# Optimization experiments

Hardware: AMD Instinct MI355X
Metric: run time of the kernel (lower is better)

## Reference

```python
import jax, jax.numpy as jnp
import numpy as np

B, C, H, W = 8, 256, 48, 48
CR = C // 8  # query/key channel dim of the 1x1 conv projections


def setup_inputs() -> dict:
    key = jax.random.key(0)
    ks = jax.random.split(key, 8)
    s = 0.05  # weight scale
    return {
        "feat_map": jax.random.normal(ks[0], (B, C, H, W), dtype=jnp.float32),
        "w1": jax.random.normal(ks[1], (CR, C), dtype=jnp.float32) * s,
        "b1": jax.random.normal(ks[2], (CR,), dtype=jnp.float32) * s,
        "w2": jax.random.normal(ks[3], (CR, C), dtype=jnp.float32) * s,
        "b2": jax.random.normal(ks[4], (CR,), dtype=jnp.float32) * s,
        "w3": jax.random.normal(ks[5], (C, C), dtype=jnp.float32) * s,
        "b3": jax.random.normal(ks[6], (C,), dtype=jnp.float32) * s,
        "gamma": jnp.asarray(0.1, dtype=jnp.float32),  # torch inits to 0; nonzero for a meaningful baseline
    }


def reference(feat_map, w1, b1, w2, b2, w3, b3, gamma):
    b, c, h, w = feat_map.shape
    n = h * w
    x = feat_map.reshape(b, c, n)                     # [B,C,N]
    # 1x1 convs == per-pixel channel matmuls
    q = jnp.einsum('dc,bcn->bnd', w1, x) + b1         # [B,N,C/8]
    k = jnp.einsum('dc,bcn->bdn', w2, x) + b2[None, :, None]  # [B,C/8,N]
    attn = jax.nn.softmax(jnp.einsum('bnd,bdm->bnm', q, k), axis=-1)  # [B,N,N]
    v = jnp.einsum('dc,bcn->bdn', w3, x) + b3[None, :, None]  # [B,C,N]
    # out[b,c,i] = sum_j v[b,c,j] * attn[b,i,j]  (matches bmm(v, attn^T))
    refine = jnp.einsum('bcj,bij->bci', v, attn).reshape(b, c, h, w)
    return gamma * refine + feat_map
```

## Files before the change

### kernel.cpp

```cpp
#include <hip/hip_runtime.h>
#include <stdint.h>

#define NB  8
#define NC  256
#define NCR 32
#define NSP 2304

typedef __attribute__((ext_vector_type(8))) short short8;
typedef __attribute__((ext_vector_type(4))) float f32x4;
typedef __attribute__((ext_vector_type(4))) unsigned short us4;

__device__ __forceinline__ unsigned short f2bf(float f) {
  union { float f; unsigned u; } a; a.f = f;
  unsigned r = (a.u + 0x7FFFu + ((a.u >> 16) & 1u)) >> 16;
  return (unsigned short)r;
}

typedef __attribute__((address_space(1))) const void* gvoidp;
typedef __attribute__((address_space(3))) void* lvoidp;
#define GLOADLDS16(g, l) __builtin_amdgcn_global_load_lds((gvoidp)(g), (lvoidp)(l), 16, 0, 0)

__global__ __launch_bounds__(256) void k_proj(const float* __restrict__ x,
    const float* __restrict__ w1, const float* __restrict__ b1,
    const float* __restrict__ w2, const float* __restrict__ b2,
    const float* __restrict__ w3, const float* __restrict__ b3,
    unsigned short* __restrict__ Q, unsigned short* __restrict__ K,
    unsigned short* __restrict__ V) {
  __shared__ unsigned short xs[32][264];
  const int n0 = blockIdx.x * 32, b = blockIdx.y;
  const int t = threadIdx.x, lane = t & 63, wave = t >> 6;
  const int col = lane & 15, quad = lane >> 4;
  const float* xb = x + (size_t)b * NC * NSP;
#pragma unroll
  for (int p = 0; p < 8; ++p) {
    const int crow = (t >> 3) + p * 32;
    const int n4 = (t & 7) * 4;
    float4 v = *(const float4*)(xb + (size_t)crow * NSP + n0 + n4);
    xs[n4 + 0][crow] = f2bf(v.x);
    xs[n4 + 1][crow] = f2bf(v.y);
    xs[n4 + 2][crow] = f2bf(v.z);
    xs[n4 + 3][crow] = f2bf(v.w);
  }
  __syncthreads();
  const f32x4 zero4 = {0.f, 0.f, 0.f, 0.f};
  f32x4 acc[5][2];
#pragma unroll
  for (int i = 0; i < 5; ++i)
#pragma unroll
    for (int j = 0; j < 2; ++j) acc[i][j] = zero4;

  for (int kc = 0; kc < 8; ++kc) {
    short8 bf[2];
#pragma unroll
    for (int nt = 0; nt < 2; ++nt)
      bf[nt] = *(const short8*)&xs[nt * 16 + col][kc * 32 + quad * 8];
#pragma unroll
    for (int ml = 0; ml < 5; ++ml) {
      const int m0 = (wave * 5 + ml) * 16;
      const float* wbase; int roff;
      if (m0 < 32)      { wbase = w1; roff = m0; }
      else if (m0 < 64) { wbase = w2; roff = m0 - 32; }
      else              { wbase = w3; roff = m0 - 64; }
      const float* wp = wbase + (size_t)(roff + col) * NC + kc * 32 + quad * 8;
      float4 f0 = *(const float4*)wp;
      float4 f1 = *(const float4*)(wp + 4);
      short8 af;
      af[0] = f2bf(f0.x); af[1] = f2bf(f0.y); af[2] = f2bf(f0.z); af[3] = f2bf(f0.w);
      af[4] = f2bf(f1.x); af[5] = f2bf(f1.y); af[6] = f2bf(f1.z); af[7] = f2bf(f1.w);
#pragma unroll
      for (int nt = 0; nt < 2; ++nt)
        acc[ml][nt] = __builtin_amdgcn_mfma_f32_16x16x32_bf16(af, bf[nt], acc[ml][nt], 0, 0, 0);
    }
  }
#pragma unroll
  for (int ml = 0; ml < 5; ++ml) {
    const int m0 = (wave * 5 + ml) * 16;
    const float* bias;
    if (m0 < 32)      bias = b1 + m0;
    else if (m0 < 64) bias = b2 + (m0 - 32);
    else              bias = b3 + (m0 - 64);
    float bv[4];
#pragma unroll
    for (int r = 0; r < 4; ++r) bv[r] = bias[quad * 4 + r];
    if (m0 < 64) {
      unsigned short* dst = (m0 < 32) ? Q : K;
      const int d0 = (m0 & 31) + quad * 4;
#pragma unroll
      for (int nt = 0; nt < 2; ++nt) {
        const int n = n0 + nt * 16 + col;
        us4 pk;
#pragma unroll
        for (int r = 0; r < 4; ++r) pk[r] = f2bf(acc[ml][nt][r] + bv[r]);
        *(us4*)(dst + ((size_t)b * NSP + n) * NCR + d0) = pk;
      }
    } else {
      const int cbase = m0 - 64 + quad * 4;
#pragma unroll
      for (int nt = 0; nt < 2; ++nt) {
        const int n = n0 + nt * 16 + col;
#pragma unroll
        for (int r = 0; r < 4; ++r)
          V[((size_t)b * NC + cbase + r) * NSP + n] = f2bf(acc[ml][nt][r] + bv[r]);
      }
    }
  }
}

__global__ __launch_bounds__(192) void k_attn(const unsigned short* __restrict__ Q,
    const unsigned short* __restrict__ K, const unsigned short* __restrict__ V,
    const float* __restrict__ feat, const float* __restrict__ gamma,
    float* __restrict__ out) {
  __shared__ __align__(16) char smem[46592];
  unsigned short* Vs = (unsigned short*)smem;
  unsigned short* Ps = (unsigned short*)(smem + 32768);
  const int i0 = blockIdx.x * 48, ch = blockIdx.y * 128, b = blockIdx.z;
  const int t = threadIdx.x, lane = t & 63, wave = t >> 6;
  const int col = lane & 15, quad = lane >> 4;
  const int iw = i0 + wave * 16;
  const unsigned short* Qb = Q + (size_t)b * NSP * NCR;
  const unsigned short* Kb = K + (size_t)b * NSP * NCR;
  const unsigned short* Vb = V + (size_t)b * NC * NSP;
  unsigned short* PsW = Ps + wave * 2304;

  const short8 qa = *(const short8*)(Qb + (size_t)(iw + col) * NCR + quad * 8);
  const f32x4 zero4 = {0.f, 0.f, 0.f, 0.f};
  f32x4 acc[8];
#pragma unroll
  for (int ct = 0; ct < 8; ++ct) acc[ct] = zero4;
  float rs[4] = {0.f, 0.f, 0.f, 0.f};
  const int srow = lane >> 2, sj = (lane & 3) * 8;

  short8 kb[4];
#pragma unroll
  for (int mt = 0; mt < 4; ++mt)
    kb[mt] = *(const short8*)(Kb + (size_t)(mt * 16 + col) * NCR + quad * 8);
#pragma unroll
  for (int cix = 0; cix < 6; ++cix) {
    const int q = wave * 6 + cix;
    if (q < 16) {
      const int kk = q >> 3, cb = (q & 7) * 16;
      const unsigned short* g = Vb + (size_t)(ch + cb + srow) * NSP + kk * 32 + sj;
      GLOADLDS16(g, Vs + kk * 4096 + cb * 32);
    }
  }
#pragma unroll
  for (int mt = 0; mt < 4; ++mt) {
    f32x4 s = __builtin_amdgcn_mfma_f32_16x16x32_bf16(qa, kb[mt], zero4, 0, 0, 0);
#pragma unroll
    for (int r = 0; r < 4; ++r) {
      const float e = __expf(s[r]);
      rs[r] += e;
      PsW[(quad * 4 + r) * 72 + mt * 16 + col] = f2bf(e);
    }
  }

  for (int kc = 0; kc < 36; ++kc) {
    __syncthreads();
    const int bufc = kc & 1, bufn = bufc ^ 1;
    const int j1 = (kc + 1) * 64;
    const bool more = (kc + 1 < 36);
    if (more) {
#pragma unroll
      for (int mt = 0; mt < 4; ++mt)
        kb[mt] = *(const short8*)(Kb + (size_t)(j1 + mt * 16 + col) * NCR + quad * 8);
#pragma unroll
      for (int cix = 0; cix < 6; ++cix) {
        const int q = wave * 6 + cix;
        if (q < 16) {
          const int kk = q >> 3, cb = (q & 7) * 16;
          const unsigned short* g = Vb + (size_t)(ch + cb + srow) * NSP + j1 + kk * 32 + sj;
          GLOADLDS16(g, Vs + bufn * 8192 + kk * 4096 + cb * 32);
        }
      }
    }
    const unsigned short* pwc = PsW + bufc * 1152;
    const unsigned short* vsc = Vs + bufc * 8192;
#pragma unroll
    for (int kk = 0; kk < 2; ++kk) {
      const short8 pa = *(const short8*)(pwc + col * 72 + kk * 32 + quad * 8);
#pragma unroll
      for (int ct = 0; ct < 8; ++ct) {
        const short8 vbf = *(const short8*)(vsc + kk * 4096 + (ct * 16 + col) * 32 + quad * 8);
        acc[ct] = __builtin_amdgcn_mfma_f32_16x16x32_bf16(pa, vbf, acc[ct], 0, 0, 0);
      }
    }
    if (more) {
      unsigned short* pwn = PsW + bufn * 1152;
#pragma unroll
      for (int mt = 0; mt < 4; ++mt) {
        f32x4 s = __builtin_amdgcn_mfma_f32_16x16x32_bf16(qa, kb[mt], zero4, 0, 0, 0);
#pragma unroll
        for (int r = 0; r < 4; ++r) {
          const float e = __expf(s[r]);
          rs[r] += e;
          pwn[(quad * 4 + r) * 72 + mt * 16 + col] = f2bf(e);
        }
      }
    }
  }

#pragma unroll
  for (int off = 1; off < 16; off <<= 1)
#pragma unroll
    for (int r = 0; r < 4; ++r) rs[r] += __shfl_xor(rs[r], off, 64);
  const float g = gamma[0];
  float rinv[4];
#pragma unroll
  for (int r = 0; r < 4; ++r) rinv[r] = g / rs[r];

  const float* fb = feat + (size_t)b * NC * NSP;
  float* ob = out + (size_t)b * NC * NSP;
#pragma unroll
  for (int ct = 0; ct < 8; ++ct) {
    const size_t a0 = (size_t)(ch + ct * 16 + col) * NSP + iw + quad * 4;
    float4 f = *(const float4*)(fb + a0);
    float4 o;
    o.x = acc[ct][0] * rinv[0] + f.x;
    o.y = acc[ct][1] * rinv[1] + f.y;
    o.z = acc[ct][2] * rinv[2] + f.z;
    o.w = acc[ct][3] * rinv[3] + f.w;
    *(float4*)(ob + a0) = o;
  }
}

#define OFF_Q  0UL
#define OFF_K  1179648UL
#define OFF_V  2359296UL

extern "C" void kernel_launch(void* const* d_in, const int* in_sizes, int n_in,
                              void* d_out, int out_size, void* d_ws, size_t ws_size,
                              hipStream_t stream) {
  const float* feat  = (const float*)d_in[0];
  const float* w1    = (const float*)d_in[1];
  const float* b1    = (const float*)d_in[2];
  const float* w2    = (const float*)d_in[3];
  const float* b2    = (const float*)d_in[4];
  const float* w3    = (const float*)d_in[5];
  const float* b3    = (const float*)d_in[6];
  const float* gamma = (const float*)d_in[7];
  float* out = (float*)d_out;
  char* ws = (char*)d_ws;
  unsigned short* Q = (unsigned short*)(ws + OFF_Q);
  unsigned short* K = (unsigned short*)(ws + OFF_K);
  unsigned short* V = (unsigned short*)(ws + OFF_V);

  hipLaunchKernelGGL(k_proj, dim3(72, NB), dim3(256), 0, stream,
                     feat, w1, b1, w2, b2, w3, b3, Q, K, V);
  hipLaunchKernelGGL(k_attn, dim3(48, 2, NB), dim3(192), 0, stream,
                     Q, K, V, feat, gamma, out);
}
```

Measured before the change: 171.0 us.

## Retile attention kernel to 96 queries x 64 channels with XOR-swizzled V tiles

Each wave now handles two 16-row query tiles against 64 channels instead of one tile against 128 channels. Each V fragment read from LDS therefore feeds two MFMAs, halving V LDS traffic per MFMA. The V tile is stored in a new 64-wide row layout with XOR swizzling to avoid LDS bank conflicts. The trade-off is that each block recomputes QK^T and exp for twice as many queries, across four channel blocks instead of two. That doubles the redundant softmax work, in exchange for less LDS use and better V reuse.

```diff
diff --git a/kernel.cpp b/kernel.cpp
--- a/kernel.cpp
+++ b/kernel.cpp
@@ -110,49 +110,55 @@
     const unsigned short* __restrict__ K, const unsigned short* __restrict__ V,
     const float* __restrict__ feat, const float* __restrict__ gamma,
     float* __restrict__ out) {
-  __shared__ __align__(16) char smem[46592];
-  unsigned short* Vs = (unsigned short*)smem;
-  unsigned short* Ps = (unsigned short*)(smem + 32768);
-  const int i0 = blockIdx.x * 48, ch = blockIdx.y * 128, b = blockIdx.z;
+  __shared__ __align__(16) unsigned short smem[22016];
+  unsigned short* Vs = smem;
+  unsigned short* Ps = smem + 8192;
+  const int i0 = blockIdx.x * 96, ch = blockIdx.y * 64, b = blockIdx.z;
   const int t = threadIdx.x, lane = t & 63, wave = t >> 6;
   const int col = lane & 15, quad = lane >> 4;
-  const int iw = i0 + wave * 16;
+  const int iw = i0 + wave * 32;
   const unsigned short* Qb = Q + (size_t)b * NSP * NCR;
   const unsigned short* Kb = K + (size_t)b * NSP * NCR;
   const unsigned short* Vb = V + (size_t)b * NC * NSP;
-  unsigned short* PsW = Ps + wave * 2304;
-
-  const short8 qa = *(const short8*)(Qb + (size_t)(iw + col) * NCR + quad * 8);
+  unsigned short* PsW = Ps + wave * 4608;
+
+  short8 qa[2];
+#pragma unroll
+  for (int it = 0; it < 2; ++it)
+    qa[it] = *(const short8*)(Qb + (size_t)(iw + it * 16 + col) * NCR + quad * 8);
   const f32x4 zero4 = {0.f, 0.f, 0.f, 0.f};
-  f32x4 acc[8];
-#pragma unroll
-  for (int ct = 0; ct < 8; ++ct) acc[ct] = zero4;
-  float rs[4] = {0.f, 0.f, 0.f, 0.f};
-  const int srow = lane >> 2, sj = (lane & 3) * 8;
+  f32x4 acc[2][4];
+#pragma unroll
+  for (int it = 0; it < 2; ++it)
+#pragma unroll
+    for (int ct = 0; ct < 4; ++ct) acc[it][ct] = zero4;
+  float rs[2][4] = {{0.f,0.f,0.f,0.f},{0.f,0.f,0.f,0.f}};
+  const int r8 = lane >> 3, pc = lane & 7, jcs = pc ^ r8;
 
   short8 kb[4];
 #pragma unroll
   for (int mt = 0; mt < 4; ++mt)
     kb[mt] = *(const short8*)(Kb + (size_t)(mt * 16 + col) * NCR + quad * 8);
 #pragma unroll
-  for (int cix = 0; cix < 6; ++cix) {
-    const int q = wave * 6 + cix;
-    if (q < 16) {
-      const int kk = q >> 3, cb = (q & 7) * 16;
-      const unsigned short* g = Vb + (size_t)(ch + cb + srow) * NSP + kk * 32 + sj;
-      GLOADLDS16(g, Vs + kk * 4096 + cb * 32);
-    }
-  }
-#pragma unroll
-  for (int mt = 0; mt < 4; ++mt) {
-    f32x4 s = __builtin_amdgcn_mfma_f32_16x16x32_bf16(qa, kb[mt], zero4, 0, 0, 0);
-#pragma unroll
-    for (int r = 0; r < 4; ++r) {
-      const float e = __expf(s[r]);
-      rs[r] += e;
-      PsW[(quad * 4 + r) * 72 + mt * 16 + col] = f2bf(e);
-    }
-  }
+  for (int cix = 0; cix < 3; ++cix) {
+    const int q = wave * 3 + cix;
+    if (q < 8) {
+      const unsigned short* g = Vb + (size_t)(ch + q * 8 + r8) * NSP + jcs * 8;
+      GLOADLDS16(g, Vs + q * 512);
+    }
+  }
+#pragma unroll
+  for (int it = 0; it < 2; ++it)
+#pragma unroll
+    for (int mt = 0; mt < 4; ++mt) {
+      f32x4 s = __builtin_amdgcn_mfma_f32_16x16x32_bf16(qa[it], kb[mt], zero4, 0, 0, 0);
+#pragma unroll
+      for (int r = 0; r < 4; ++r) {
+        const float e = __expf(s[r]);
+        rs[it][r] += e;
+        PsW[(it * 16 + quad * 4 + r) * 72 + mt * 16 + col] = f2bf(e);
+      }
+    }
 
   for (int kc = 0; kc < 36; ++kc) {
     __syncthreads();
@@ -164,63 +170,75 @@
       for (int mt = 0; mt < 4; ++mt)
         kb[mt] = *(const short8*)(Kb + (size_t)(j1 + mt * 16 + col) * NCR + quad * 8);
 #pragma unroll
-      for (int cix = 0; cix < 6; ++cix) {
-        const int q = wave * 6 + cix;
-        if (q < 16) {
-          const int kk = q >> 3, cb = (q & 7) * 16;
-          const unsigned short* g = Vb + (size_t)(ch + cb + srow) * NSP + j1 + kk * 32 + sj;
-          GLOADLDS16(g, Vs + bufn * 8192 + kk * 4096 + cb * 32);
+      for (int cix = 0; cix < 3; ++cix) {
+        const int q = wave * 3 + cix;
+        if (q < 8) {
+          const unsigned short* g = Vb + (size_t)(ch + q * 8 + r8) * NSP + j1 + jcs * 8;
+          GLOADLDS16(g, Vs + bufn * 4096 + q * 512);
         }
       }
     }
-    const unsigned short* pwc = PsW + bufc * 1152;
-    const unsigned short* vsc = Vs + bufc * 8192;
+    const unsigned short* pwc = PsW + bufc * 2304;
+    const unsigned short* vsc = Vs + bufc * 4096;
 #pragma unroll
     for (int kk = 0; kk < 2; ++kk) {
-      const short8 pa = *(const short8*)(pwc + col * 72 + kk * 32 + quad * 8);
-#pragma unroll
-      for (int ct = 0; ct < 8; ++ct) {
-        const short8 vbf = *(const short8*)(vsc + kk * 4096 + (ct * 16 + col) * 32 + quad * 8);
-        acc[ct] = __builtin_amdgcn_mfma_f32_16x16x32_bf16(pa, vbf, acc[ct], 0, 0, 0);
+      short8 pa[2];
+#pragma unroll
+      for (int it = 0; it < 2; ++it)
+        pa[it] = *(const short8*)(pwc + (it * 16 + col) * 72 + kk * 32 + quad * 8);
+#pragma unroll
+      for (int ct = 0; ct < 4; ++ct) {
+        const short8 vbf = *(const short8*)(vsc + (ct * 16 + col) * 64 +
+                                            (((kk * 4 + quad) ^ (col & 7)) * 8));
+        acc[0][ct] = __builtin_amdgcn_mfma_f32_16x16x32_bf16(pa[0], vbf, acc[0][ct], 0, 0, 0);
+        acc[1][ct] = __builtin_amdgcn_mfma_f32_16x16x32_bf16(pa[1], vbf, acc[1][ct], 0, 0, 0);
       }
     }
     if (more) {
-      unsigned short* pwn = PsW + bufn * 1152;
-#pragma unroll
-      for (int mt = 0; mt < 4; ++mt) {
-        f32x4 s = __builtin_amdgcn_mfma_f32_16x16x32_bf16(qa, kb[mt], zero4, 0, 0, 0);
-#pragma unroll
-        for (int r = 0; r < 4; ++r) {
-          const float e = __expf(s[r]);
-          rs[r] += e;
-          pwn[(quad * 4 + r) * 72 + mt * 16 + col] = f2bf(e);
+      unsigned short* pwn = PsW + bufn * 2304;
+#pragma unroll
+      for (int it = 0; it < 2; ++it)
+#pragma unroll
+        for (int mt = 0; mt < 4; ++mt) {
+          f32x4 s = __builtin_amdgcn_mfma_f32_16x16x32_bf16(qa[it], kb[mt], zero4, 0, 0, 0);
+#pragma unroll
+          for (int r = 0; r < 4; ++r) {
+            const float e = __expf(s[r]);
+            rs[it][r] += e;
+            pwn[(it * 16 + quad * 4 + r) * 72 + mt * 16 + col] = f2bf(e);
+          }
         }
-      }
     }
   }
 
 #pragma unroll
   for (int off = 1; off < 16; off <<= 1)
 #pragma unroll
-    for (int r = 0; r < 4; ++r) rs[r] += __shfl_xor(rs[r], off, 64);
+    for (int it = 0; it < 2; ++it)
+#pragma unroll
+      for (int r = 0; r < 4; ++r) rs[it][r] += __shfl_xor(rs[it][r], off, 64);
   const float g = gamma[0];
-  float rinv[4];
-#pragma unroll
-  for (int r = 0; r < 4; ++r) rinv[r] = g / rs[r];
+  float rinv[2][4];
+#pragma unroll
+  for (int it = 0; it < 2; ++it)
+#pragma unroll
+    for (int r = 0; r < 4; ++r) rinv[it][r] = g / rs[it][r];
 
   const float* fb = feat + (size_t)b * NC * NSP;
   float* ob = out + (size_t)b * NC * NSP;
 #pragma unroll
-  for (int ct = 0; ct < 8; ++ct) {
-    const size_t a0 = (size_t)(ch + ct * 16 + col) * NSP + iw + quad * 4;
-    float4 f = *(const float4*)(fb + a0);
-    float4 o;
-    o.x = acc[ct][0] * rinv[0] + f.x;
-    o.y = acc[ct][1] * rinv[1] + f.y;
-    o.z = acc[ct][2] * rinv[2] + f.z;
-    o.w = acc[ct][3] * rinv[3] + f.w;
-    *(float4*)(ob + a0) = o;
-  }
+  for (int it = 0; it < 2; ++it)
+#pragma unroll
+    for (int ct = 0; ct < 4; ++ct) {
+      const size_t a0 = (size_t)(ch + ct * 16 + col) * NSP + iw + it * 16 + quad * 4;
+      float4 f = *(const float4*)(fb + a0);
+      float4 o;
+      o.x = acc[it][ct][0] * rinv[it][0] + f.x;
+      o.y = acc[it][ct][1] * rinv[it][1] + f.y;
+      o.z = acc[it][ct][2] * rinv[it][2] + f.z;
+      o.w = acc[it][ct][3] * rinv[it][3] + f.w;
+      *(float4*)(ob + a0) = o;
+    }
 }
 
 #define OFF_Q  0UL
@@ -246,6 +264,6 @@
 
   hipLaunchKernelGGL(k_proj, dim3(72, NB), dim3(256), 0, stream,
                      feat, w1, b1, w2, b2, w3, b3, Q, K, V);
-  hipLaunchKernelGGL(k_attn, dim3(48, 2, NB), dim3(192), 0, stream,
+  hipLaunchKernelGGL(k_attn, dim3(24, 4, NB), dim3(192), 0, stream,
                      Q, K, V, feat, gamma, out);
 }
```

Result: slower. 182.0 us (+6.5%).
